# Performance work log

Measured on AMD Instinct MI355X. Metric: run time of the kernel, lower is better.

Reference implementation:

```python
import jax, jax.numpy as jnp
import numpy as np

# db4 reconstruction filters (pywt convention): rec_lo = reversed(dec_lo),
# rec_hi[k] = (-1)^k * dec_lo[k]
REC_LO = [0.23037781330885523, 0.7148465705525415, 0.6308807679295904,
          -0.02798376941698385, -0.18703481171888114, 0.030841381835986965,
          0.032883011666982945, -0.010597401784997278]
REC_HI = [-0.010597401784997278, -0.032883011666982945, 0.030841381835986965,
          0.18703481171888114, -0.02798376941698385, -0.6308807679295904,
          0.7148465705525415, -0.23037781330885523]
FILT_LEN = 8


def _idwt1d(cA, cD, axis):
    """Periodized single-level inverse DWT along `axis`. N -> 2N."""
    cA = jnp.moveaxis(cA, axis, -1)
    cD = jnp.moveaxis(cD, axis, -1)
    N = cA.shape[-1]
    up_a = jnp.zeros(cA.shape[:-1] + (2 * N,), cA.dtype).at[..., ::2].set(cA)
    up_d = jnp.zeros(cD.shape[:-1] + (2 * N,), cD.dtype).at[..., ::2].set(cD)
    # circular synthesis: y[m] = sum_k g[k]*up_a[m-k] + h[k]*up_d[m-k]
    y = sum(REC_LO[k] * jnp.roll(up_a, k, axis=-1) +
            REC_HI[k] * jnp.roll(up_d, k, axis=-1) for k in range(FILT_LEN))
    y = jnp.roll(y, -(FILT_LEN - 2), axis=-1)  # phase alignment (periodization)
    return jnp.moveaxis(y, -1, axis)


def setup_inputs() -> dict:
    key = jax.random.key(0)
    x = jax.random.normal(key, (64, 256, 256, 16), dtype=jnp.float32)
    return {"x": x}


def reference(x):
    # x: [B, H, W, 4*C] with channel groups = (cA, cH, cV, cD)
    c = x.shape[-1] // 4
    cA, cH, cV, cD = (x[..., :c], x[..., c:2 * c],
                      x[..., 2 * c:3 * c], x[..., 3 * c:])
    lo = _idwt1d(cA, cH, axis=1)   # [B, 2H, W, C]
    hi = _idwt1d(cV, cD, axis=1)   # [B, 2H, W, C]
    return _idwt1d(lo, hi, axis=2)  # [B, 2H, 2W, C]
```

## Files before the change

### kernel.cpp

```cpp
#include <hip/hip_runtime.h>
#include <hip/hip_bf16.h>


#define N 256
#define RJ 16

#define LGKM_BARRIER()                                   \
  do {                                                   \
    asm volatile("s_waitcnt lgkmcnt(0)" ::: "memory");   \
    __builtin_amdgcn_s_barrier();                        \
    asm volatile("" ::: "memory");                       \
  } while (0)

__device__ __forceinline__ void fma4(float4& d, float s, const float4 a) {
  d.x = fmaf(s, a.x, d.x);
  d.y = fmaf(s, a.y, d.y);
  d.z = fmaf(s, a.z, d.z);
  d.w = fmaf(s, a.w, d.w);
}

__device__ __forceinline__ uint2 pack_bf16x4(const float4 v) {
  __hip_bfloat162 lo = __float22bfloat162_rn(make_float2(v.x, v.y));
  __hip_bfloat162 hi = __float22bfloat162_rn(make_float2(v.z, v.w));
  uint2 r;
  r.x = *reinterpret_cast<const unsigned int*>(&lo);
  r.y = *reinterpret_cast<const unsigned int*>(&hi);
  return r;
}

__device__ __forceinline__ float4 unpack_bf16x4(const uint2 u) {
  float4 r;
  r.x = __uint_as_float(u.x << 16);
  r.y = __uint_as_float(u.x & 0xffff0000u);
  r.z = __uint_as_float(u.y << 16);
  r.w = __uint_as_float(u.y & 0xffff0000u);
  return r;
}

__global__ __launch_bounds__(512, 4) void idwt2_sep11_kernel(
    const float* __restrict__ x, float* __restrict__ out) {
  constexpr float LO[8] = {
      0.23037781330885523f,  0.7148465705525415f,  0.6308807679295904f,
      -0.02798376941698385f, -0.18703481171888114f, 0.030841381835986965f,
      0.032883011666982945f, -0.010597401784997278f};
  constexpr float HIW[8] = {
      -0.010597401784997278f, -0.032883011666982945f, 0.030841381835986965f,
      0.18703481171888114f,  -0.02798376941698385f,  -0.6308807679295904f,
      0.7148465705525415f,   -0.23037781330885523f};
  const float Lw[2][4] = {{LO[6], LO[4], LO[2], LO[0]},
                          {LO[7], LO[5], LO[3], LO[1]}};
  const float Hw[2][4] = {{HIW[6], HIW[4], HIW[2], HIW[0]},
                          {HIW[7], HIW[5], HIW[3], HIW[1]}};

  __shared__ uint2 I[2][2][2][N];

  const int t = threadIdx.x;
  const int bx = blockIdx.x;
  const int b = bx >> 4;
  const int r0 = (bx & 15) * RJ;

  const float4* xb = reinterpret_cast<const float4*>(x) + (size_t)b * N * N * 4;
  float4* ob = reinterpret_cast<float4*>(out) + (size_t)b * (2 * N) * (2 * N);

  const int tcol = t >> 1;
  const int thalf = t & 1;
  const float4* xcolp = xb + (size_t)t * 2;

  float4 wA[4], wB[4], nA, nB;
  auto ldrow = [&](int lr, float4& A, float4& B) {
    const int gr = (r0 + lr) & (N - 1);
    A = xcolp[(size_t)gr * (N * 4)];
    B = xcolp[(size_t)gr * (N * 4) + 1];
  };

  auto p1 = [&](int j, int buf) {
    float4 v0 = make_float4(0.f, 0.f, 0.f, 0.f);
    float4 v1 = make_float4(0.f, 0.f, 0.f, 0.f);
#pragma unroll
    for (int sy = 0; sy < 4; ++sy) {
      const float4 a = wA[(j + sy) & 3];
      const float4 bb = wB[(j + sy) & 3];
      fma4(v0, Lw[0][sy], a);
      fma4(v0, Hw[0][sy], bb);
      fma4(v1, Lw[1][sy], a);
      fma4(v1, Hw[1][sy], bb);
    }
    I[buf][0][thalf][tcol] = pack_bf16x4(v0);
    I[buf][1][thalf][tcol] = pack_bf16x4(v1);
  };

#pragma unroll
  for (int m = 0; m < 4; ++m) ldrow(m, wA[m], wB[m]);
  ldrow(4, nA, nB);
  p1(0, 0);
  wA[0] = nA;
  wB[0] = nB;
  ldrow(5, nA, nB);
  LGKM_BARRIER();

  const int jx = t >> 1;
  const int q = t & 1;
  float Lq[4], Hq[4];
#pragma unroll
  for (int s = 0; s < 4; ++s) {
    Lq[s] = q ? Lw[1][s] : Lw[0][s];
    Hq[s] = q ? Hw[1][s] : Hw[0][s];
  }

#pragma unroll
  for (int c = 0; c < RJ; ++c) {
    const int buf = c & 1;

    float4 o0 = make_float4(0.f, 0.f, 0.f, 0.f);
    float4 o1 = make_float4(0.f, 0.f, 0.f, 0.f);
#pragma unroll
    for (int s = 0; s < 4; ++s) {
      const int xc = (jx + s) & (N - 1);
      const float4 l0 = unpack_bf16x4(I[buf][0][0][xc]);
      const float4 h0 = unpack_bf16x4(I[buf][0][1][xc]);
      const float4 l1 = unpack_bf16x4(I[buf][1][0][xc]);
      const float4 h1 = unpack_bf16x4(I[buf][1][1][xc]);
      fma4(o0, Lq[s], l0);
      fma4(o0, Hq[s], h0);
      fma4(o1, Lq[s], l1);
      fma4(o1, Hq[s], h1);
    }
    const int jy = r0 + c;
    float4* po = ob + (size_t)(2 * jy) * (2 * N) + t;
    po[0] = o0;
    po[2 * N] = o1;

    if (c < RJ - 1) {
      p1(c + 1, buf ^ 1);
      if (c <= RJ - 3) {
        wA[(c + 1) & 3] = nA;
        wB[(c + 1) & 3] = nB;
      }
      if (c <= RJ - 4) ldrow(c + 6, nA, nB);
      LGKM_BARRIER();
    }
  }
}

extern "C" void kernel_launch(void* const* d_in, const int* in_sizes, int n_in,
                              void* d_out, int out_size, void* d_ws,
                              size_t ws_size, hipStream_t stream) {
  const float* x = reinterpret_cast<const float*>(d_in[0]);
  float* out = reinterpret_cast<float*>(d_out);
  const int grid = 64 * (N / RJ);
  idwt2_sep11_kernel<<<grid, 512, 0, stream>>>(x, out);
}
```

Measured before the change: 111.0 us.

## Halve rows per block, remap thread-to-column split, use vector FMA types

```diff
diff --git a/kernel.cpp b/kernel.cpp
--- a/kernel.cpp
+++ b/kernel.cpp
@@ -3,7 +3,9 @@
 
 
 #define N 256
-#define RJ 16
+#define RJ 8
+
+typedef float f32x4 __attribute__((ext_vector_type(4)));
 
 #define LGKM_BARRIER()                                   \
   do {                                                   \
@@ -12,14 +14,13 @@
     asm volatile("" ::: "memory");                       \
   } while (0)
 
-__device__ __forceinline__ void fma4(float4& d, float s, const float4 a) {
-  d.x = fmaf(s, a.x, d.x);
-  d.y = fmaf(s, a.y, d.y);
-  d.z = fmaf(s, a.z, d.z);
-  d.w = fmaf(s, a.w, d.w);
+__device__ __forceinline__ f32x4 fma4v(const f32x4 acc, const float s,
+                                       const f32x4 a) {
+  const f32x4 sv = {s, s, s, s};
+  return __builtin_elementwise_fma(a, sv, acc);
 }
 
-__device__ __forceinline__ uint2 pack_bf16x4(const float4 v) {
+__device__ __forceinline__ uint2 pack_bf16x4(const f32x4 v) {
   __hip_bfloat162 lo = __float22bfloat162_rn(make_float2(v.x, v.y));
   __hip_bfloat162 hi = __float22bfloat162_rn(make_float2(v.z, v.w));
   uint2 r;
@@ -28,8 +29,8 @@
   return r;
 }
 
-__device__ __forceinline__ float4 unpack_bf16x4(const uint2 u) {
-  float4 r;
+__device__ __forceinline__ f32x4 unpack_bf16x4(const uint2 u) {
+  f32x4 r;
   r.x = __uint_as_float(u.x << 16);
   r.y = __uint_as_float(u.x & 0xffff0000u);
   r.z = __uint_as_float(u.y << 16);
@@ -37,7 +38,7 @@
   return r;
 }
 
-__global__ __launch_bounds__(512, 4) void idwt2_sep11_kernel(
+__global__ __launch_bounds__(512, 4) void idwt2_sep12_kernel(
     const float* __restrict__ x, float* __restrict__ out) {
   constexpr float LO[8] = {
       0.23037781330885523f,  0.7148465705525415f,  0.6308807679295904f,
@@ -56,34 +57,34 @@
 
   const int t = threadIdx.x;
   const int bx = blockIdx.x;
-  const int b = bx >> 4;
-  const int r0 = (bx & 15) * RJ;
+  const int b = bx >> 5;
+  const int r0 = (bx & 31) * RJ;
 
-  const float4* xb = reinterpret_cast<const float4*>(x) + (size_t)b * N * N * 4;
-  float4* ob = reinterpret_cast<float4*>(out) + (size_t)b * (2 * N) * (2 * N);
+  const f32x4* xb = reinterpret_cast<const f32x4*>(x) + (size_t)b * N * N * 4;
+  f32x4* ob = reinterpret_cast<f32x4*>(out) + (size_t)b * (2 * N) * (2 * N);
 
-  const int tcol = t >> 1;
-  const int thalf = t & 1;
-  const float4* xcolp = xb + (size_t)t * 2;
+  const int tcol = t & (N - 1);
+  const int thalf = t >> 8;
+  const f32x4* xcolp = xb + (size_t)tcol * 4 + thalf * 2;
 
-  float4 wA[4], wB[4], nA, nB;
-  auto ldrow = [&](int lr, float4& A, float4& B) {
+  f32x4 wA[4], wB[4], nA, nB;
+  auto ldrow = [&](int lr, f32x4& A, f32x4& B) {
     const int gr = (r0 + lr) & (N - 1);
     A = xcolp[(size_t)gr * (N * 4)];
     B = xcolp[(size_t)gr * (N * 4) + 1];
   };
 
   auto p1 = [&](int j, int buf) {
-    float4 v0 = make_float4(0.f, 0.f, 0.f, 0.f);
-    float4 v1 = make_float4(0.f, 0.f, 0.f, 0.f);
+    f32x4 v0 = {0.f, 0.f, 0.f, 0.f};
+    f32x4 v1 = {0.f, 0.f, 0.f, 0.f};
 #pragma unroll
     for (int sy = 0; sy < 4; ++sy) {
-      const float4 a = wA[(j + sy) & 3];
-      const float4 bb = wB[(j + sy) & 3];
-      fma4(v0, Lw[0][sy], a);
-      fma4(v0, Hw[0][sy], bb);
-      fma4(v1, Lw[1][sy], a);
-      fma4(v1, Hw[1][sy], bb);
+      const f32x4 a = wA[(j + sy) & 3];
+      const f32x4 bb = wB[(j + sy) & 3];
+      v0 = fma4v(v0, Lw[0][sy], a);
+      v0 = fma4v(v0, Hw[0][sy], bb);
+      v1 = fma4v(v1, Lw[1][sy], a);
+      v1 = fma4v(v1, Hw[1][sy], bb);
     }
     I[buf][0][thalf][tcol] = pack_bf16x4(v0);
     I[buf][1][thalf][tcol] = pack_bf16x4(v1);
@@ -111,22 +112,22 @@
   for (int c = 0; c < RJ; ++c) {
     const int buf = c & 1;
 
-    float4 o0 = make_float4(0.f, 0.f, 0.f, 0.f);
-    float4 o1 = make_float4(0.f, 0.f, 0.f, 0.f);
+    f32x4 o0 = {0.f, 0.f, 0.f, 0.f};
+    f32x4 o1 = {0.f, 0.f, 0.f, 0.f};
 #pragma unroll
     for (int s = 0; s < 4; ++s) {
       const int xc = (jx + s) & (N - 1);
-      const float4 l0 = unpack_bf16x4(I[buf][0][0][xc]);
-      const float4 h0 = unpack_bf16x4(I[buf][0][1][xc]);
-      const float4 l1 = unpack_bf16x4(I[buf][1][0][xc]);
-      const float4 h1 = unpack_bf16x4(I[buf][1][1][xc]);
-      fma4(o0, Lq[s], l0);
-      fma4(o0, Hq[s], h0);
-      fma4(o1, Lq[s], l1);
-      fma4(o1, Hq[s], h1);
+      const f32x4 l0 = unpack_bf16x4(I[buf][0][0][xc]);
+      const f32x4 h0 = unpack_bf16x4(I[buf][0][1][xc]);
+      const f32x4 l1 = unpack_bf16x4(I[buf][1][0][xc]);
+      const f32x4 h1 = unpack_bf16x4(I[buf][1][1][xc]);
+      o0 = fma4v(o0, Lq[s], l0);
+      o0 = fma4v(o0, Hq[s], h0);
+      o1 = fma4v(o1, Lq[s], l1);
+      o1 = fma4v(o1, Hq[s], h1);
     }
     const int jy = r0 + c;
-    float4* po = ob + (size_t)(2 * jy) * (2 * N) + t;
+    f32x4* po = ob + (size_t)(2 * jy) * (2 * N) + t;
     po[0] = o0;
     po[2 * N] = o1;
 
@@ -148,5 +149,5 @@
   const float* x = reinterpret_cast<const float*>(d_in[0]);
   float* out = reinterpret_cast<float*>(d_out);
   const int grid = 64 * (N / RJ);
-  idwt2_sep11_kernel<<<grid, 512, 0, stream>>>(x, out);
+  idwt2_sep12_kernel<<<grid, 512, 0, stream>>>(x, out);
 }
```

Result: slower. 122.6 us (+10.4%).
